# Performance work log

Measured on AMD Instinct MI355X. Metric: run time of the kernel, lower is better.

The kernel has to match this reference:

```python
import jax, jax.numpy as jnp
import numpy as np

B, T, DM = 2, 2048, 2048
HQ, HKV, D = 16, 4, 128
MULT = 0.08838834764831845  # attn_output_multiplier = 1/sqrt(key_size)
ROPE_BASE = 10000.0


def rotate_half(x):
    x1, x2 = jnp.split(x, 2, axis=-1)
    return jnp.concatenate((-x2, x1), axis=-1)


def rope_tables(seq_len, dim, dtype):
    inv_freq = 1.0 / (ROPE_BASE ** (jnp.arange(0, dim, 2, dtype=jnp.float32) / dim))
    t = jnp.arange(seq_len, dtype=jnp.float32)
    freqs = jnp.outer(t, inv_freq)              # [T, D/2]
    emb = jnp.concatenate((freqs, freqs), axis=-1)  # [T, D]
    cos = jnp.cos(emb)[None, :, None, :].astype(dtype)  # [1, T, 1, D]
    sin = jnp.sin(emb)[None, :, None, :].astype(dtype)
    return cos, sin


def setup_inputs() -> dict:
    key = jax.random.key(0)
    ks = jax.random.split(key, 5)
    s = 1.0 / np.sqrt(DM)
    x = jax.random.normal(ks[0], (B, T, DM), dtype=jnp.float32)
    Wq = jax.random.normal(ks[1], (DM, HQ * D), dtype=jnp.float32) * s
    Wk = jax.random.normal(ks[2], (DM, HKV * D), dtype=jnp.float32) * s
    Wv = jax.random.normal(ks[3], (DM, HKV * D), dtype=jnp.float32) * s
    Wo = jax.random.normal(ks[4], (HQ * D, DM), dtype=jnp.float32) * s
    mask = jnp.tril(jnp.ones((T, T), dtype=bool))[None, None]  # [1,1,T,T] causal
    return {"x": x, "mask": mask, "Wq": Wq, "Wk": Wk, "Wv": Wv, "Wo": Wo}


def reference(x, mask, Wq, Wk, Wv, Wo):
    Bx, Tx, _ = x.shape
    q = (x @ Wq).reshape(Bx, Tx, HQ, D)
    k = (x @ Wk).reshape(Bx, Tx, HKV, D)
    v = (x @ Wv).reshape(Bx, Tx, HKV, D)
    cos, sin = rope_tables(Tx, D, x.dtype)
    q = q * cos + rotate_half(q) * sin
    k = k * cos + rotate_half(k) * sin
    n_rep = HQ // HKV
    k = jnp.repeat(k, n_rep, axis=2)  # [B,T,HQ,D] (repeat_interleave)
    v = jnp.repeat(v, n_rep, axis=2)
    logits = jnp.einsum('bqhd,bkhd->bhqk', q, k) * MULT
    logits = jnp.where(mask, logits, jnp.float32(-jnp.inf))
    attn = jax.nn.softmax(logits.astype(jnp.float32), axis=-1).astype(x.dtype)
    out = jnp.einsum('bhqk,bkhd->bqhd', attn, v).reshape(Bx, Tx, HQ * D)
    return out @ Wo
```

## Files before the change

kernel.cpp:

```cpp
#include <hip/hip_runtime.h>
#include <cstdint>
#include <cstddef>

#define T_SEQ 2048
#define DMODEL 2048
#define HQ 16
#define HKV 4
#define HD 128

typedef __attribute__((ext_vector_type(4))) float f32x4;
typedef __attribute__((ext_vector_type(8))) short bf16x8;
typedef __attribute__((ext_vector_type(4))) short short4v;
typedef __attribute__((ext_vector_type(2))) short short2v;
typedef __attribute__((ext_vector_type(4))) unsigned uint4v;

__device__ __forceinline__ short f2bf(float f) {
  unsigned u = __builtin_bit_cast(unsigned, f);
  u = (u + 0x7FFFu + ((u >> 16) & 1u)) >> 16;
  return (short)u;
}
__device__ __forceinline__ float bf2f(short s) {
  unsigned u = ((unsigned)(unsigned short)s) << 16;
  return __builtin_bit_cast(float, u);
}
__device__ __forceinline__ unsigned pk_hi16(float a, float b) {
  return __builtin_amdgcn_perm(__builtin_bit_cast(unsigned, b),
                               __builtin_bit_cast(unsigned, a), 0x07060302u);
}

__device__ __forceinline__ void g2lds16(const void* g, void* l) {
  __builtin_amdgcn_global_load_lds(
      (const __attribute__((address_space(1))) void*)g,
      (__attribute__((address_space(3))) void*)l, 16, 0, 0);
}

__global__ void cvt_kernel(const float* __restrict__ src, short* __restrict__ dst, int n) {
  int idx = blockIdx.x * 256 + threadIdx.x;
  int i = idx * 4;
  if (i >= n) return;
  float4 v = *(const float4*)(src + i);
  short4v o;
  o[0] = f2bf(v.x); o[1] = f2bf(v.y); o[2] = f2bf(v.z); o[3] = f2bf(v.w);
  *(short4v*)(dst + i) = o;
}

__global__ void transpose_cvt4(const float* __restrict__ s0, const float* __restrict__ s1,
                               const float* __restrict__ s2, const float* __restrict__ s3,
                               short* __restrict__ d0, short* __restrict__ d1,
                               short* __restrict__ d2, short* __restrict__ d3) {
  __shared__ float tile[32][33];
  const int z = blockIdx.z;
  const float* src = (z == 0) ? s0 : (z == 1) ? s1 : (z == 2) ? s2 : s3;
  short* dst = (z == 0) ? d0 : (z == 1) ? d1 : (z == 2) ? d2 : d3;
  const int C = (z == 1 || z == 2) ? 512 : 2048;
  const int R = 2048;
  int c0 = blockIdx.x * 32, r0 = blockIdx.y * 32;
  if (c0 >= C) return;
  int tx = threadIdx.x, ty = threadIdx.y;
  #pragma unroll
  for (int i = 0; i < 32; i += 8)
    tile[ty + i][tx] = src[(size_t)(r0 + ty + i) * C + c0 + tx];
  __syncthreads();
  #pragma unroll
  for (int i = 0; i < 32; i += 8)
    dst[(size_t)(c0 + ty + i) * R + r0 + tx] = f2bf(tile[tx][ty + i]);
}

template <int MODE>
__global__ __launch_bounds__(256, 2) void gemm_kernel(
    const short* __restrict__ A, const short* __restrict__ BT,
    void* __restrict__ C0, void* __restrict__ C1, void* __restrict__ C2,
    int M, int N, int K)
{
  __shared__ short As[128 * 32];
  __shared__ short Bs[128 * 32];
  const int tid = threadIdx.x;
  const int lane = tid & 63, w = tid >> 6;
  const int l15 = lane & 15, g = lane >> 4;
  const int m0 = blockIdx.y * 128, n0 = blockIdx.x * 128;
  const int wm = (w >> 1) * 64, wn = (w & 1) * 64;

  f32x4 acc[4][4] = {};

  for (int k0 = 0; k0 < K; k0 += 32) {
    __syncthreads();
    #pragma unroll
    for (int call = 0; call < 2; call++) {
      int tau = call * 256 + tid;
      int row = tau >> 2, c = tau & 3;
      int swz = (row & 3) ^ ((row >> 2) & 3);
      g2lds16(A + (size_t)(m0 + row) * K + k0 + ((c ^ swz) << 3),
              (char*)As + call * 4096 + w * 1024);
      g2lds16(BT + (size_t)(n0 + row) * K + k0 + ((c ^ swz) << 3),
              (char*)Bs + call * 4096 + w * 1024);
    }
    __syncthreads();
    bf16x8 af[4], bfr[4];
    #pragma unroll
    for (int mi = 0; mi < 4; mi++) {
      int row = wm + mi * 16 + l15;
      int ch = g ^ ((row & 3) ^ ((row >> 2) & 3));
      af[mi] = *(const bf16x8*)(As + row * 32 + ch * 8);
    }
    #pragma unroll
    for (int ni = 0; ni < 4; ni++) {
      int row = wn + ni * 16 + l15;
      int ch = g ^ ((row & 3) ^ ((row >> 2) & 3));
      bfr[ni] = *(const bf16x8*)(Bs + row * 32 + ch * 8);
    }
    #pragma unroll
    for (int mi = 0; mi < 4; mi++)
      #pragma unroll
      for (int ni = 0; ni < 4; ni++)
        acc[mi][ni] = __builtin_amdgcn_mfma_f32_16x16x32_bf16(af[mi], bfr[ni], acc[mi][ni], 0, 0, 0);
  }

  if (MODE == 1) {
    float* C = (float*)C0;
    #pragma unroll
    for (int mi = 0; mi < 4; mi++)
      #pragma unroll
      for (int r = 0; r < 4; r++) {
        int m = m0 + wm + mi * 16 + g * 4 + r;
        #pragma unroll
        for (int ni = 0; ni < 4; ni++)
          C[(size_t)m * N + n0 + wn + ni * 16 + l15] = acc[mi][ni][r];
      }
  } else {
    short* Cb; int ldc, nc;
    if (MODE == 0) { Cb = (short*)C0; ldc = N; nc = n0; }
    else {
      if (n0 < 2048)      { Cb = (short*)C0; ldc = 2048; nc = n0; }
      else if (n0 < 2560) { Cb = (short*)C1; ldc = 512;  nc = n0 - 2048; }
      else                { Cb = (short*)C2; ldc = 512;  nc = n0 - 2560; }
    }
    #pragma unroll
    for (int mi = 0; mi < 4; mi++)
      #pragma unroll
      for (int r = 0; r < 4; r++) {
        int m = m0 + wm + mi * 16 + g * 4 + r;
        #pragma unroll
        for (int ni = 0; ni < 4; ni++)
          Cb[(size_t)m * ldc + nc + wn + ni * 16 + l15] = f2bf(acc[mi][ni][r]);
      }
  }
}

__global__ void rope_all(short* __restrict__ qbuf, short* __restrict__ kbuf, float qscale) {
  int idx = blockIdx.x * 256 + threadIdx.x;
  short* buf; int NH; float scale;
  if (idx < 4194304) { buf = qbuf; NH = HQ; scale = qscale; }
  else               { buf = kbuf; NH = HKV; scale = 1.0f; idx -= 4194304; }
  int i = idx & 63;
  int th = idx >> 6;
  int t = (th / NH) % T_SEQ;
  size_t base = (size_t)th * 128;
  float invf = exp2f(-(float)i * 0.20762050593046014f);
  float theta = (float)t * invf;
  float sn, cs;
  sincosf(theta, &sn, &cs);
  float a = bf2f(buf[base + i]);
  float b = bf2f(buf[base + 64 + i]);
  buf[base + i]      = f2bf((a * cs - b * sn) * scale);
  buf[base + 64 + i] = f2bf((b * cs + a * sn) * scale);
}

__global__ __launch_bounds__(512, 4) void attn_kernel(
    const short* __restrict__ qg, const short* __restrict__ kg,
    const short* __restrict__ vg, short* __restrict__ og)
{
  __shared__ short Ks[2][64 * 128];
  __shared__ short Vt[128 * 64];
  const int tid = threadIdx.x;
  const int lane = tid & 63, w = tid >> 6;
  const int l15 = lane & 15, g = lane >> 4;
  const int b = blockIdx.z;
  const int qti = b ? (15 - (int)blockIdx.x) : (int)blockIdx.x;
  const int qt0 = qti * 128;
  const int h = blockIdx.y, hk = h >> 2;
  const int qw0 = qt0 + w * 16;

  bf16x8 qf[4];
  {
    size_t t = (size_t)b * T_SEQ + qw0 + l15;
    const short* qp = qg + (t * HQ + h) * HD;
    #pragma unroll
    for (int ks = 0; ks < 4; ks++)
      qf[ks] = *(const bf16x8*)(qp + ks * 32 + g * 8);
  }

  f32x4 of[8] = {};
  float m2 = -INFINITY;
  float ls = 0.f;

  const short* kbase = kg + ((size_t)b * T_SEQ * HKV + hk) * HD;
  const short* vbase = vg + ((size_t)b * T_SEQ * HKV + hk) * HD;

  const int kv2 = (tid & 31) * 2;
  const int d8s = (tid >> 5) * 8;
  const int p0 = (kv2 >> 5) * 32 + ((kv2 & 15) >> 2) * 8 + ((kv2 >> 4) & 1) * 4 + (kv2 & 3);
  const int nt = (qt0 + 128) >> 6;

  bf16x8 vr[2];

  auto stageK = [&](int t, int nb) {
    #pragma unroll
    for (int call = 0; call < 2; call++) {
      int tau = call * 512 + tid;
      int kv = tau >> 4, c = tau & 15;
      g2lds16(kbase + (size_t)(t * 64 + kv) * (HKV * HD) + ((c ^ (kv & 7)) << 3),
              (char*)Ks[nb] + call * 8192 + w * 1024);
    }
  };
  auto loadV = [&](int t) {
    const short* vp = vbase + (size_t)(t * 64 + kv2) * (HKV * HD) + d8s;
    vr[0] = *(const bf16x8*)(vp);
    vr[1] = *(const bf16x8*)(vp + HKV * HD);
  };
  auto writeV = [&]() {
    #pragma unroll
    for (int e = 0; e < 8; e++) {
      int row = d8s + e;
      int addr = row * 64 + (((p0 >> 3) ^ e) << 3) + (p0 & 7);
      short2v t2; t2[0] = vr[0][e]; t2[1] = vr[1][e];
      *(short2v*)(&Vt[addr]) = t2;
    }
  };

  stageK(0, 0);
  loadV(0);
  __syncthreads();
  writeV();
  __syncthreads();

  int cur = 0;
  for (int t = 0; t < nt; t++) {
    const int kv0 = t * 64;
    const bool haveNext = (t + 1 < nt);
    if (haveNext) { loadV(t + 1); stageK(t + 1, cur ^ 1); }

    if (kv0 <= qw0 + 15) {
      const short* Kc = Ks[cur];
      f32x4 sacc[4] = {};
      __builtin_amdgcn_s_setprio(1);
      #pragma unroll
      for (int ks = 0; ks < 4; ks++) {
        bf16x8 kf[4];
        #pragma unroll
        for (int kt = 0; kt < 4; kt++) {
          int row = kt * 16 + l15;
          int ch = (ks * 4 + g) ^ (row & 7);
          kf[kt] = *(const bf16x8*)(Kc + row * 128 + ch * 8);
        }
        #pragma unroll
        for (int kt = 0; kt < 4; kt++)
          sacc[kt] = __builtin_amdgcn_mfma_f32_16x16x32_bf16(kf[kt], qf[ks], sacc[kt], 0, 0, 0);
      }
      __builtin_amdgcn_s_setprio(0);
      const bool needmask = (kv0 + 63) > qw0;
      const int qpos = qw0 + l15;
      float vmax = -INFINITY;
      #pragma unroll
      for (int kt = 0; kt < 4; kt++)
        #pragma unroll
        for (int r = 0; r < 4; r++) {
          int kvpos = kv0 + kt * 16 + g * 4 + r;
          float sv = sacc[kt][r];
          if (needmask && kvpos > qpos) sv = -INFINITY;
          sacc[kt][r] = sv;
          vmax = fmaxf(vmax, sv);
        }
      vmax = fmaxf(vmax, __shfl_xor(vmax, 16));
      vmax = fmaxf(vmax, __shfl_xor(vmax, 32));
      if (!__all(vmax <= m2 + 8.0f)) {
        float mnew = fmaxf(m2, vmax);
        float resc = exp2f(m2 - mnew);
        m2 = mnew;
        ls *= resc;
        #pragma unroll
        for (int dc = 0; dc < 8; dc++) of[dc] *= resc;
      }
      float lsum = 0.f;
      #pragma unroll
      for (int kt = 0; kt < 4; kt++)
        #pragma unroll
        for (int r = 0; r < 4; r++) {
          float p = exp2f(sacc[kt][r] - m2);
          sacc[kt][r] = p;
          lsum += p;
        }
      lsum += __shfl_xor(lsum, 16);
      lsum += __shfl_xor(lsum, 32);
      ls += lsum;
      bf16x8 pb[2];
      #pragma unroll
      for (int ktw = 0; ktw < 2; ktw++) {
        uint4v pw;
        pw[0] = pk_hi16(sacc[2 * ktw][0], sacc[2 * ktw][1]);
        pw[1] = pk_hi16(sacc[2 * ktw][2], sacc[2 * ktw][3]);
        pw[2] = pk_hi16(sacc[2 * ktw + 1][0], sacc[2 * ktw + 1][1]);
        pw[3] = pk_hi16(sacc[2 * ktw + 1][2], sacc[2 * ktw + 1][3]);
        pb[ktw] = __builtin_bit_cast(bf16x8, pw);
      }
      __builtin_amdgcn_s_setprio(1);
      #pragma unroll
      for (int ktw = 0; ktw < 2; ktw++)
        #pragma unroll
        for (int dc = 0; dc < 8; dc++) {
          int row = dc * 16 + l15;
          bf16x8 vf = *(const bf16x8*)(&Vt[row * 64 + ((ktw * 32 + g * 8) ^ ((l15 & 7) << 3))]);
          of[dc] = __builtin_amdgcn_mfma_f32_16x16x32_bf16(vf, pb[ktw], of[dc], 0, 0, 0);
        }
      __builtin_amdgcn_s_setprio(0);
    }

    __syncthreads();
    if (haveNext) writeV();
    __syncthreads();
    cur ^= 1;
  }

  {
    float inv = 1.0f / ls;
    size_t t = (size_t)b * T_SEQ + qw0 + l15;
    short* op = og + (t * HQ + h) * HD;
    #pragma unroll
    for (int dc = 0; dc < 8; dc++) {
      short4v o;
      #pragma unroll
      for (int r = 0; r < 4; r++) o[r] = f2bf(of[dc][r] * inv);
      *(short4v*)(op + dc * 16 + g * 4) = o;
    }
  }
}

extern "C" void kernel_launch(void* const* d_in, const int* in_sizes, int n_in,
                              void* d_out, int out_size, void* d_ws, size_t ws_size,
                              hipStream_t stream) {
  (void)in_sizes; (void)n_in; (void)out_size; (void)ws_size;
  const float* x  = (const float*)d_in[0];
  const float* Wq = (const float*)d_in[2];
  const float* Wk = (const float*)d_in[3];
  const float* Wv = (const float*)d_in[4];
  const float* Wo = (const float*)d_in[5];

  char* ws = (char*)d_ws;
  short* xb   = (short*)(ws);
  short* wall = (short*)(ws + 16777216);
  short* wkT  = wall + (size_t)2048 * 2048;
  short* wvT  = wall + (size_t)2560 * 2048;
  short* woT  = (short*)(ws + 29360128);
  short* qb   = (short*)(ws + 37748736);
  short* kb   = (short*)(ws + 54525952);
  short* vb   = (short*)(ws + 58720256);
  short* ab   = (short*)(ws + 62914560);

  const float MULT = 0.08838834764831845f;
  const float LOG2E = 1.4426950408889634f;
  const float QSCALE = MULT * LOG2E;

  dim3 tb(32, 8);
  cvt_kernel<<<8192, 256, 0, stream>>>(x, xb, 8388608);
  transpose_cvt4<<<dim3(64, 64, 4), tb, 0, stream>>>(Wq, Wk, Wv, Wo, wall, wkT, wvT, woT);

  gemm_kernel<2><<<dim3(24, 32), 256, 0, stream>>>(xb, wall, qb, kb, vb, 4096, 3072, 2048);

  rope_all<<<20480, 256, 0, stream>>>(qb, kb, QSCALE);

  attn_kernel<<<dim3(16, 16, 2), 512, 0, stream>>>(qb, kb, vb, ab);

  gemm_kernel<1><<<dim3(16, 32), 256, 0, stream>>>(ab, woT, d_out, nullptr, nullptr, 4096, 2048, 2048);
}
```

Measured before the change: 225.0 us.

## Replace GEMM with 256x128 tile, BK=64 double-buffered pipelined kernel

Replaces the 128x128 single-buffered GEMM (BK=32, two full barriers per k-step) with a 512-thread 256x128 tile kernel. It uses BK=64 and double-buffered LDS, with global-to-LDS prefetch two k-steps ahead interleaved into four MFMA phases. Phases are separated by raw s_barrier plus sched_barrier, with setprio raised around MFMA bursts. The goal is to hide load latency and cut barrier overhead for both the QKV and output projections. The cost is a new swizzled LDS layout, a hand-tuned vmcnt wait, a smaller grid and lower occupancy.

```diff
diff --git a/kernel.cpp b/kernel.cpp
--- a/kernel.cpp
+++ b/kernel.cpp
@@ -13,6 +13,9 @@
 typedef __attribute__((ext_vector_type(4))) short short4v;
 typedef __attribute__((ext_vector_type(2))) short short2v;
 typedef __attribute__((ext_vector_type(4))) unsigned uint4v;
+
+#define SBAR() __builtin_amdgcn_s_barrier()
+#define SFEN() __builtin_amdgcn_sched_barrier(0)
 
 __device__ __forceinline__ short f2bf(float f) {
   unsigned u = __builtin_bit_cast(unsigned, f);
@@ -67,52 +70,131 @@
 }
 
 template <int MODE>
-__global__ __launch_bounds__(256, 2) void gemm_kernel(
+__global__ __launch_bounds__(512, 1) void gemm256(
     const short* __restrict__ A, const short* __restrict__ BT,
     void* __restrict__ C0, void* __restrict__ C1, void* __restrict__ C2,
     int M, int N, int K)
 {
-  __shared__ short As[128 * 32];
-  __shared__ short Bs[128 * 32];
+  __shared__ short As[2][256 * 64];
+  __shared__ short Bs[2][128 * 64];
   const int tid = threadIdx.x;
-  const int lane = tid & 63, w = tid >> 6;
+  const int lane = tid & 63, wid = tid >> 6;
   const int l15 = lane & 15, g = lane >> 4;
-  const int m0 = blockIdx.y * 128, n0 = blockIdx.x * 128;
-  const int wm = (w >> 1) * 64, wn = (w & 1) * 64;
+  const int wr = wid >> 1, wc = wid & 1;
+  const int bm0 = blockIdx.y * 256, bn0 = blockIdx.x * 128;
+
+  const int qloc = (wid & 3) * 64 + lane;
+  const int r_in = ((qloc >> 7) << 4) + ((qloc >> 2) & 15);
+  const int c8s  = (((qloc >> 6) & 1) << 2) +
+                   ((qloc & 3) ^ ((((qloc >> 2) & 15) >> 3) << 1));
+  const int wg   = wid >> 2;
+  const int ldsl = (wid & 3) * 1024;
+
+  const int rdoff = l15 * 4 + (g ^ ((l15 >> 3) << 1));
+
+  auto stageA = [&](int c, int k0, int nb) {
+    int row0 = (c < 2) ? ((c * 2 + wg) * 64) : (((c - 2) * 2 + wg) * 64 + 32);
+    g2lds16(A + (size_t)(bm0 + row0 + r_in) * K + k0 + c8s * 8,
+            (char*)As[nb] + row0 * 128 + ldsl);
+  };
+  auto stageB = [&](int c, int k0, int nb) {
+    int row0 = wg * 64 + c * 32;
+    g2lds16(BT + (size_t)(bn0 + row0 + r_in) * K + k0 + c8s * 8,
+            (char*)Bs[nb] + row0 * 128 + ldsl);
+  };
+  auto readA = [&](int mi, int kk, int nb) -> bf16x8 {
+    int p = ((wr * 4 + mi) * 2 + kk) * 64 + rdoff;
+    return *(const bf16x8*)((const char*)As[nb] + p * 16);
+  };
+  auto readB = [&](int ni, int kk, int nb) -> bf16x8 {
+    int p = ((wc * 4 + ni) * 2 + kk) * 64 + rdoff;
+    return *(const bf16x8*)((const char*)Bs[nb] + p * 16);
+  };
 
   f32x4 acc[4][4] = {};
-
-  for (int k0 = 0; k0 < K; k0 += 32) {
-    __syncthreads();
-    #pragma unroll
-    for (int call = 0; call < 2; call++) {
-      int tau = call * 256 + tid;
-      int row = tau >> 2, c = tau & 3;
-      int swz = (row & 3) ^ ((row >> 2) & 3);
-      g2lds16(A + (size_t)(m0 + row) * K + k0 + ((c ^ swz) << 3),
-              (char*)As + call * 4096 + w * 1024);
-      g2lds16(BT + (size_t)(n0 + row) * K + k0 + ((c ^ swz) << 3),
-              (char*)Bs + call * 4096 + w * 1024);
-    }
-    __syncthreads();
-    bf16x8 af[4], bfr[4];
-    #pragma unroll
-    for (int mi = 0; mi < 4; mi++) {
-      int row = wm + mi * 16 + l15;
-      int ch = g ^ ((row & 3) ^ ((row >> 2) & 3));
-      af[mi] = *(const bf16x8*)(As + row * 32 + ch * 8);
-    }
-    #pragma unroll
-    for (int ni = 0; ni < 4; ni++) {
-      int row = wn + ni * 16 + l15;
-      int ch = g ^ ((row & 3) ^ ((row >> 2) & 3));
-      bfr[ni] = *(const bf16x8*)(Bs + row * 32 + ch * 8);
-    }
-    #pragma unroll
-    for (int mi = 0; mi < 4; mi++)
-      #pragma unroll
-      for (int ni = 0; ni < 4; ni++)
-        acc[mi][ni] = __builtin_amdgcn_mfma_f32_16x16x32_bf16(af[mi], bfr[ni], acc[mi][ni], 0, 0, 0);
+  const int nk = K >> 6;
+
+  #pragma unroll
+  for (int c = 0; c < 4; c++) stageA(c, 0, 0);
+  #pragma unroll
+  for (int c = 0; c < 2; c++) stageB(c, 0, 0);
+  #pragma unroll
+  for (int c = 0; c < 4; c++) stageA(c, 64, 1);
+  #pragma unroll
+  for (int c = 0; c < 2; c++) stageB(c, 64, 1);
+  asm volatile("s_waitcnt vmcnt(6)" ::: "memory");
+  SFEN(); SBAR(); SFEN();
+
+  for (int t = 0; t < nk; t++) {
+    const int nb = t & 1;
+    const int kp = (t + 2) << 6;
+    const bool pre = (t + 2) < nk;
+    bf16x8 aLO[2][2], aHI[2][2], bLO[2][2], bHI[2][2];
+
+    #pragma unroll
+    for (int mi = 0; mi < 2; mi++)
+      #pragma unroll
+      for (int kk = 0; kk < 2; kk++) aLO[mi][kk] = readA(mi, kk, nb);
+    #pragma unroll
+    for (int ni = 0; ni < 2; ni++)
+      #pragma unroll
+      for (int kk = 0; kk < 2; kk++) bLO[ni][kk] = readB(ni, kk, nb);
+    __builtin_amdgcn_s_setprio(1);
+    #pragma unroll
+    for (int kk = 0; kk < 2; kk++)
+      #pragma unroll
+      for (int mi = 0; mi < 2; mi++)
+        #pragma unroll
+        for (int ni = 0; ni < 2; ni++)
+          acc[mi][ni] = __builtin_amdgcn_mfma_f32_16x16x32_bf16(aLO[mi][kk], bLO[ni][kk], acc[mi][ni], 0, 0, 0);
+    __builtin_amdgcn_s_setprio(0);
+    SFEN(); SBAR(); SFEN();
+
+    #pragma unroll
+    for (int ni = 0; ni < 2; ni++)
+      #pragma unroll
+      for (int kk = 0; kk < 2; kk++) bHI[ni][kk] = readB(ni + 2, kk, nb);
+    if (pre) { stageA(0, kp, nb); stageA(1, kp, nb); stageB(0, kp, nb); }
+    __builtin_amdgcn_s_setprio(1);
+    #pragma unroll
+    for (int kk = 0; kk < 2; kk++)
+      #pragma unroll
+      for (int mi = 0; mi < 2; mi++)
+        #pragma unroll
+        for (int ni = 0; ni < 2; ni++)
+          acc[mi][ni + 2] = __builtin_amdgcn_mfma_f32_16x16x32_bf16(aLO[mi][kk], bHI[ni][kk], acc[mi][ni + 2], 0, 0, 0);
+    __builtin_amdgcn_s_setprio(0);
+    SFEN(); SBAR(); SFEN();
+
+    #pragma unroll
+    for (int mi = 0; mi < 2; mi++)
+      #pragma unroll
+      for (int kk = 0; kk < 2; kk++) aHI[mi][kk] = readA(mi + 2, kk, nb);
+    if (pre) stageB(1, kp, nb);
+    __builtin_amdgcn_s_setprio(1);
+    #pragma unroll
+    for (int kk = 0; kk < 2; kk++)
+      #pragma unroll
+      for (int mi = 0; mi < 2; mi++)
+        #pragma unroll
+        for (int ni = 0; ni < 2; ni++)
+          acc[mi + 2][ni] = __builtin_amdgcn_mfma_f32_16x16x32_bf16(aHI[mi][kk], bLO[ni][kk], acc[mi + 2][ni], 0, 0, 0);
+    __builtin_amdgcn_s_setprio(0);
+    SFEN(); SBAR(); SFEN();
+
+    if (pre) { stageA(2, kp, nb); stageA(3, kp, nb); }
+    __builtin_amdgcn_s_setprio(1);
+    #pragma unroll
+    for (int kk = 0; kk < 2; kk++)
+      #pragma unroll
+      for (int mi = 0; mi < 2; mi++)
+        #pragma unroll
+        for (int ni = 0; ni < 2; ni++)
+          acc[mi + 2][ni + 2] = __builtin_amdgcn_mfma_f32_16x16x32_bf16(aHI[mi][kk], bHI[ni][kk], acc[mi + 2][ni + 2], 0, 0, 0);
+    __builtin_amdgcn_s_setprio(0);
+    if (pre) { asm volatile("s_waitcnt vmcnt(6)" ::: "memory"); }
+    else     { asm volatile("s_waitcnt vmcnt(0)" ::: "memory"); }
+    SFEN(); SBAR(); SFEN();
   }
 
   if (MODE == 1) {
@@ -121,27 +203,24 @@
     for (int mi = 0; mi < 4; mi++)
       #pragma unroll
       for (int r = 0; r < 4; r++) {
-        int m = m0 + wm + mi * 16 + g * 4 + r;
+        int m = bm0 + wr * 64 + mi * 16 + g * 4 + r;
         #pragma unroll
         for (int ni = 0; ni < 4; ni++)
-          C[(size_t)m * N + n0 + wn + ni * 16 + l15] = acc[mi][ni][r];
+          C[(size_t)m * N + bn0 + wc * 64 + ni * 16 + l15] = acc[mi][ni][r];
       }
   } else {
     short* Cb; int ldc, nc;
-    if (MODE == 0) { Cb = (short*)C0; ldc = N; nc = n0; }
-    else {
-      if (n0 < 2048)      { Cb = (short*)C0; ldc = 2048; nc = n0; }
-      else if (n0 < 2560) { Cb = (short*)C1; ldc = 512;  nc = n0 - 2048; }
-      else                { Cb = (short*)C2; ldc = 512;  nc = n0 - 2560; }
-    }
+    if (bn0 < 2048)      { Cb = (short*)C0; ldc = 2048; nc = bn0; }
+    else if (bn0 < 2560) { Cb = (short*)C1; ldc = 512;  nc = bn0 - 2048; }
+    else                 { Cb = (short*)C2; ldc = 512;  nc = bn0 - 2560; }
     #pragma unroll
     for (int mi = 0; mi < 4; mi++)
       #pragma unroll
       for (int r = 0; r < 4; r++) {
-        int m = m0 + wm + mi * 16 + g * 4 + r;
+        int m = bm0 + wr * 64 + mi * 16 + g * 4 + r;
         #pragma unroll
         for (int ni = 0; ni < 4; ni++)
-          Cb[(size_t)m * ldc + nc + wn + ni * 16 + l15] = f2bf(acc[mi][ni][r]);
+          Cb[(size_t)m * ldc + nc + wc * 64 + ni * 16 + l15] = f2bf(acc[mi][ni][r]);
       }
   }
 }
@@ -363,11 +442,11 @@
   cvt_kernel<<<8192, 256, 0, stream>>>(x, xb, 8388608);
   transpose_cvt4<<<dim3(64, 64, 4), tb, 0, stream>>>(Wq, Wk, Wv, Wo, wall, wkT, wvT, woT);
 
-  gemm_kernel<2><<<dim3(24, 32), 256, 0, stream>>>(xb, wall, qb, kb, vb, 4096, 3072, 2048);
+  gemm256<2><<<dim3(24, 16), 512, 0, stream>>>(xb, wall, qb, kb, vb, 4096, 3072, 2048);
 
   rope_all<<<20480, 256, 0, stream>>>(qb, kb, QSCALE);
 
   attn_kernel<<<dim3(16, 16, 2), 512, 0, stream>>>(qb, kb, vb, ab);
 
-  gemm_kernel<1><<<dim3(16, 32), 256, 0, stream>>>(ab, woT, d_out, nullptr, nullptr, 4096, 2048, 2048);
-}
+  gemm256<1><<<dim3(16, 16), 512, 0, stream>>>(ab, woT, d_out, nullptr, nullptr, 4096, 2048, 2048);
+}
```

Measured after the change: 255.2 us. +13.5%, slower.
